# Optimization experiments

Hardware: AMD Instinct MI355X
Metric: run time of the kernel (lower is better)

Reference implementation:

```python
import jax, jax.numpy as jnp
import numpy as np

N_NODES = 100_000
N_EDGES = 1_600_000
N_GRAPHS = 2048
IN_CH, HID, EMB = 6, 64, 16
N_LIG, N_ADD, N_BASE, N_ARYL = 12, 23, 4, 16
TOTAL_IN = HID + 4 * EMB  # 128


def setup_inputs() -> dict:
    key = jax.random.key(0)
    ks = jax.random.split(key, 20)
    p = lambda k, shape: (jax.random.normal(k, shape, jnp.float32) * 0.05)
    return {
        "x": jax.random.normal(ks[0], (N_NODES, IN_CH), jnp.float32),
        "edge_index": jax.random.randint(ks[1], (2, N_EDGES), 0, N_NODES),
        "batch": jnp.sort(jax.random.randint(ks[2], (N_NODES,), 0, N_GRAPHS)),
        "ligand_idx": jax.random.randint(ks[3], (N_GRAPHS,), 0, N_LIG),
        "additive_idx": jax.random.randint(ks[4], (N_GRAPHS,), 0, N_ADD),
        "base_idx": jax.random.randint(ks[5], (N_GRAPHS,), 0, N_BASE),
        "aryl_idx": jax.random.randint(ks[6], (N_GRAPHS,), 0, N_ARYL),
        "emb_ligand": p(ks[7], (N_LIG, EMB)),
        "emb_additive": p(ks[8], (N_ADD, EMB)),
        "emb_base": p(ks[9], (N_BASE, EMB)),
        "emb_aryl": p(ks[10], (N_ARYL, EMB)),
        "W1": p(ks[11], (IN_CH, HID)),
        "b1": jnp.zeros((HID,), jnp.float32),
        "W2": p(ks[12], (HID, HID)),
        "b2": jnp.zeros((HID,), jnp.float32),
        "lin1_W": p(ks[13], (TOTAL_IN, HID)),
        "lin1_b": jnp.zeros((HID,), jnp.float32),
        "lin2_W": p(ks[14], (HID, 1)),
        "lin2_b": jnp.zeros((1,), jnp.float32),
    }


def gcn_conv(x, src, dst, W, b):
    """PyG GCNConv: add self-loops, sym-normalize, aggregate xW over edges."""
    n = x.shape[0]
    xw = x @ W  # [N, out]
    loop = jnp.arange(n)
    s = jnp.concatenate([src, loop])
    d = jnp.concatenate([dst, loop])
    deg = jax.ops.segment_sum(jnp.ones_like(d, dtype=xw.dtype), d, num_segments=n)
    dinv = jax.lax.rsqrt(jnp.maximum(deg, 1.0))  # deg >= 1 due to self-loops
    norm = (dinv[s] * dinv[d])[:, None]
    return jax.ops.segment_sum(xw[s] * norm, d, num_segments=n) + b


def reference(x, edge_index, batch, ligand_idx, additive_idx, base_idx, aryl_idx,
              emb_ligand, emb_additive, emb_base, emb_aryl,
              W1, b1, W2, b2, lin1_W, lin1_b, lin2_W, lin2_b):
    src, dst = edge_index[0], edge_index[1]
    h = jax.nn.relu(gcn_conv(x, src, dst, W1, b1))
    h = jax.nn.relu(gcn_conv(h, src, dst, W2, b2))
    # global mean pool over graphs
    sums = jax.ops.segment_sum(h, batch, num_segments=N_GRAPHS)
    cnt = jax.ops.segment_sum(jnp.ones((h.shape[0],), h.dtype), batch, num_segments=N_GRAPHS)
    pooled = sums / jnp.maximum(cnt, 1.0)[:, None]  # [G, HID]
    cat = jnp.concatenate([
        pooled,
        emb_ligand[ligand_idx], emb_additive[additive_idx],
        emb_base[base_idx], emb_aryl[aryl_idx],
    ], axis=-1)  # [G, HID + 4*EMB]
    hmid = jax.nn.relu(cat @ lin1_W + lin1_b)  # dropout is identity in eval mode
    return hmid @ lin2_W + lin2_b  # [G, 1]
```

## Files before the change

kernel.cpp:

```cpp
#include <hip/hip_runtime.h>
#include <hip/hip_bf16.h>

#define PCHUNK 4096
#define NBK 1024
#define BSZ 128
#define CAP 2560
#define CNT_STRIDE 16

__device__ inline float bf2f(unsigned int u16) { return __uint_as_float(u16 << 16); }
__device__ inline unsigned short f2bf(float f) {
    __hip_bfloat16 b = __float2bfloat16(f);
    return *(unsigned short*)&b;
}

typedef __attribute__((ext_vector_type(8))) short v8s;
typedef __attribute__((ext_vector_type(4))) float v4f;

__global__ void k_partition(const int* __restrict__ src, const int* __restrict__ dst, int E,
                            int* __restrict__ bucket_cnt, unsigned int* __restrict__ buckets,
                            float* __restrict__ zero_base, int zero_count) {
    __shared__ int hist[NBK];
    __shared__ int shift[NBK];
    __shared__ int cursor[NBK];
    __shared__ unsigned int staged_e[PCHUNK];
    __shared__ unsigned short staged_b[PCHUNK];
    __shared__ int wtot[4];
    int t = threadIdx.x;
    int lane = t & 63, wave = t >> 6;
    int base = blockIdx.x * PCHUNK;
    for (int i = blockIdx.x * 256 + t; i < zero_count; i += gridDim.x * 256)
        zero_base[i] = 0.f;
    for (int i = t; i < NBK; i += 256) hist[i] = 0;
    __syncthreads();
    int nE = E - base; if (nE > PCHUNK) nE = PCHUNK;
    for (int i = t; i < nE; i += 256) atomicAdd(&hist[dst[base + i] >> 7], 1);
    __syncthreads();
    int h0 = hist[4 * t], h1 = hist[4 * t + 1], h2 = hist[4 * t + 2], h3 = hist[4 * t + 3];
    int p1 = h0 + h1, p2 = p1 + h2, s = p2 + h3;
    int si = s;
    #pragma unroll
    for (int off = 1; off < 64; off <<= 1) {
        int u = __shfl_up(si, off, 64);
        if (lane >= off) si += u;
    }
    if (lane == 63) wtot[wave] = si;
    __syncthreads();
    int woff = 0;
    #pragma unroll
    for (int w2 = 0; w2 < 4; ++w2) woff += (w2 < wave) ? wtot[w2] : 0;
    int ebase = woff + si - s;
    int ex[4] = {ebase, ebase + h0, ebase + p1, ebase + p2};
    int cn[4] = {h0, h1, h2, h3};
    #pragma unroll
    for (int j = 0; j < 4; ++j) {
        int bidx = 4 * t + j;
        cursor[bidx] = ex[j];
        if (cn[j] > 0) {
            int g = atomicAdd(&bucket_cnt[bidx * CNT_STRIDE], cn[j]);
            shift[bidx] = g - ex[j];
        }
    }
    __syncthreads();
    for (int i = t; i < nE; i += 256) {
        int d = dst[base + i];
        int b = d >> 7;
        int r = atomicAdd(&cursor[b], 1);
        staged_e[r] = (unsigned int)src[base + i] | ((unsigned int)(d & (BSZ - 1)) << 24);
        staged_b[r] = (unsigned short)b;
    }
    __syncthreads();
    for (int i = t; i < nE; i += 256) {
        int b = staged_b[i];
        buckets[(size_t)b * CAP + shift[b] + i] = staged_e[i];
    }
}

__global__ void k_bucket_csr_xw1(const unsigned int* __restrict__ buckets,
                                 const int* __restrict__ bucket_cnt,
                                 int* __restrict__ offs, int* __restrict__ deg,
                                 float* __restrict__ dinv, int* __restrict__ csr,
                                 const float* __restrict__ x, const float* __restrict__ W1,
                                 unsigned short* __restrict__ A, int N) {
    __shared__ int dl[BSZ], cur[BSZ];
    __shared__ float dis[BSZ];
    __shared__ float W1s[6 * 64];
    __shared__ float xs[BSZ * 6];
    __shared__ int w0tot;
    int b = blockIdx.x, t = threadIdx.x;
    int nb0 = b * BSZ;
    for (int i = t; i < 6 * 64; i += 256) W1s[i] = W1[i];
    for (int i = t; i < BSZ * 6; i += 256) {
        int node = nb0 + i / 6;
        xs[i] = (node < N) ? x[(size_t)nb0 * 6 + i] : 0.f;
    }
    if (t < BSZ) dl[t] = 0;
    __syncthreads();
    int cnt = bucket_cnt[b * CNT_STRIDE];
    if (cnt > CAP) cnt = CAP;
    const unsigned int* bp = buckets + (size_t)b * CAP;
    for (int i = t; i < cnt; i += 256) atomicAdd(&dl[bp[i] >> 24], 1);
    __syncthreads();
    int lane = t & 63, wave = t >> 6;
    int v = (t < BSZ) ? dl[t] : 0;
    int si = v;
    #pragma unroll
    for (int off = 1; off < 64; off <<= 1) {
        int u = __shfl_up(si, off, 64);
        if (lane >= off) si += u;
    }
    if (t == 63) w0tot = si;
    __syncthreads();
    int ex = si - v + ((wave == 1) ? w0tot : 0);
    if (t < BSZ) {
        cur[t] = ex;
        float di = rsqrtf((float)v + 1.0f);
        dis[t] = di;
        int n = nb0 + t;
        if (n < N) { offs[n] = b * CAP + ex; deg[n] = v; dinv[n] = di; }
    }
    __syncthreads();
    int* cg = csr + (size_t)b * CAP;
    for (int i = t; i < cnt; i += 256) {
        unsigned int e = bp[i];
        int r = atomicAdd(&cur[e >> 24], 1);
        cg[r] = (int)(e & 0x00FFFFFFu);
    }
    int ch = t & 63, sub = t >> 6;
    for (int nl = sub; nl < BSZ; nl += 4) {
        int node = nb0 + nl;
        if (node < N) {
            float acc = 0.f;
            #pragma unroll
            for (int k = 0; k < 6; ++k) acc += xs[nl * 6 + k] * W1s[k * 64 + ch];
            A[(size_t)node * 64 + ch] = f2bf(acc * dis[nl]);
        }
    }
}

__global__ void k_pull1_xw2(const unsigned short* __restrict__ A, const int* __restrict__ csr,
                            const int* __restrict__ offs, const int* __restrict__ deg,
                            const float* __restrict__ dinv, const float* __restrict__ bias,
                            const float* __restrict__ W2, unsigned short* __restrict__ A2,
                            int N) {
    __shared__ unsigned short Ht[16][72];
    int t = threadIdx.x;
    int lane = t & 63, wave = t >> 6;
    int q = lane >> 4, m = lane & 15;
    int cbase = wave * 16;
    v8s b0h, b0l, b1h, b1l;
    #pragma unroll
    for (int j = 0; j < 8; ++j) {
        float w0 = W2[(q * 8 + j) * 64 + cbase + m];
        unsigned short h0 = f2bf(w0);
        b0h[j] = (short)h0;
        b0l[j] = (short)f2bf(w0 - bf2f(h0));
        float w1 = W2[(32 + q * 8 + j) * 64 + cbase + m];
        unsigned short h1 = f2bf(w1);
        b1h[j] = (short)h1;
        b1l[j] = (short)f2bf(w1 - bf2f(h1));
    }
    int n0 = blockIdx.x * 16;
    int nl = wave * 4 + q;
    int n = n0 + nl;
    bool valid = n < N;
    int nc = valid ? n : N - 1;
    int base = offs[nc];
    int dg = valid ? deg[nc] : 0;
    int dgm = dg, o;
    o = __shfl_xor(dgm, 16, 64); dgm = dgm > o ? dgm : o;
    o = __shfl_xor(dgm, 32, 64); dgm = dgm > o ? dgm : o;
    uint2 su = *(const uint2*)(A + ((size_t)nc << 6) + 4 * m);
    float a0 = __uint_as_float(su.x << 16);
    float a1 = __uint_as_float(su.x & 0xffff0000u);
    float a2 = __uint_as_float(su.y << 16);
    float a3 = __uint_as_float(su.y & 0xffff0000u);
    int i = 0;
    for (; i + 8 <= dgm; i += 8) {
        uint2 u[8];
        #pragma unroll
        for (int j = 0; j < 8; ++j) {
            unsigned int s = (unsigned int)csr[base + i + j];
            if (s >= (unsigned int)N) s = 0;
            u[j] = *(const uint2*)(A + ((size_t)s << 6) + 4 * m);
        }
        #pragma unroll
        for (int j = 0; j < 8; ++j) {
            unsigned int ux = (i + j < dg) ? u[j].x : 0u;
            unsigned int uy = (i + j < dg) ? u[j].y : 0u;
            a0 += __uint_as_float(ux << 16);
            a1 += __uint_as_float(ux & 0xffff0000u);
            a2 += __uint_as_float(uy << 16);
            a3 += __uint_as_float(uy & 0xffff0000u);
        }
    }
    for (; i < dgm; ++i) {
        unsigned int s = (unsigned int)csr[base + i];
        if (s >= (unsigned int)N) s = 0;
        uint2 uu = *(const uint2*)(A + ((size_t)s << 6) + 4 * m);
        unsigned int ux = (i < dg) ? uu.x : 0u;
        unsigned int uy = (i < dg) ? uu.y : 0u;
        a0 += __uint_as_float(ux << 16);
        a1 += __uint_as_float(ux & 0xffff0000u);
        a2 += __uint_as_float(uy << 16);
        a3 += __uint_as_float(uy & 0xffff0000u);
    }
    float di = valid ? dinv[n] : 0.f;
    float4 bb = *(const float4*)(bias + 4 * m);
    float v0 = fmaxf(fmaf(di, a0, bb.x), 0.f);
    float v1 = fmaxf(fmaf(di, a1, bb.y), 0.f);
    float v2 = fmaxf(fmaf(di, a2, bb.z), 0.f);
    float v3 = fmaxf(fmaf(di, a3, bb.w), 0.f);
    if (valid) {
        uint2 pk;
        pk.x = (unsigned int)f2bf(v0) | ((unsigned int)f2bf(v1) << 16);
        pk.y = (unsigned int)f2bf(v2) | ((unsigned int)f2bf(v3) << 16);
        *(uint2*)&Ht[nl][4 * m] = pk;
    }
    __syncthreads();
    union { uint4 u; v8s s; } a0u, a1u;
    a0u.u = *(const uint4*)&Ht[m][q * 8];
    a1u.u = *(const uint4*)&Ht[m][32 + q * 8];
    v4f acc = {0.f, 0.f, 0.f, 0.f};
    acc = __builtin_amdgcn_mfma_f32_16x16x32_bf16(a0u.s, b0l, acc, 0, 0, 0);
    acc = __builtin_amdgcn_mfma_f32_16x16x32_bf16(a1u.s, b1l, acc, 0, 0, 0);
    acc = __builtin_amdgcn_mfma_f32_16x16x32_bf16(a0u.s, b0h, acc, 0, 0, 0);
    acc = __builtin_amdgcn_mfma_f32_16x16x32_bf16(a1u.s, b1h, acc, 0, 0, 0);
    #pragma unroll
    for (int r = 0; r < 4; ++r) {
        int node = n0 + q * 4 + r;
        if (node < N)
            A2[(size_t)node * 64 + cbase + m] = f2bf(acc[r] * dinv[node]);
    }
}

__global__ void k_pull_pool(const unsigned short* __restrict__ A, const int* __restrict__ csr,
                            const int* __restrict__ offs, const int* __restrict__ deg,
                            const float* __restrict__ dinv, const float* __restrict__ bias,
                            const int* __restrict__ batch, float* __restrict__ pool, int N) {
    __shared__ float vt[4][4][64];
    int t = threadIdx.x;
    int lane = t & 63, wave = t >> 6;
    int q = lane >> 4, m = lane & 15;
    int n0 = blockIdx.x * 16;
    int nl = wave * 4 + q;
    int n = n0 + nl;
    bool valid = n < N;
    int nc = valid ? n : N - 1;
    int base = offs[nc];
    int dg = valid ? deg[nc] : 0;
    int dgm = dg, o;
    o = __shfl_xor(dgm, 16, 64); dgm = dgm > o ? dgm : o;
    o = __shfl_xor(dgm, 32, 64); dgm = dgm > o ? dgm : o;
    uint2 su = *(const uint2*)(A + ((size_t)nc << 6) + 4 * m);
    float a0 = __uint_as_float(su.x << 16);
    float a1 = __uint_as_float(su.x & 0xffff0000u);
    float a2 = __uint_as_float(su.y << 16);
    float a3 = __uint_as_float(su.y & 0xffff0000u);
    int i = 0;
    for (; i + 8 <= dgm; i += 8) {
        uint2 u[8];
        #pragma unroll
        for (int j = 0; j < 8; ++j) {
            unsigned int s = (unsigned int)csr[base + i + j];
            if (s >= (unsigned int)N) s = 0;
            u[j] = *(const uint2*)(A + ((size_t)s << 6) + 4 * m);
        }
        #pragma unroll
        for (int j = 0; j < 8; ++j) {
            unsigned int ux = (i + j < dg) ? u[j].x : 0u;
            unsigned int uy = (i + j < dg) ? u[j].y : 0u;
            a0 += __uint_as_float(ux << 16);
            a1 += __uint_as_float(ux & 0xffff0000u);
            a2 += __uint_as_float(uy << 16);
            a3 += __uint_as_float(uy & 0xffff0000u);
        }
    }
    for (; i < dgm; ++i) {
        unsigned int s = (unsigned int)csr[base + i];
        if (s >= (unsigned int)N) s = 0;
        uint2 uu = *(const uint2*)(A + ((size_t)s << 6) + 4 * m);
        unsigned int ux = (i < dg) ? uu.x : 0u;
        unsigned int uy = (i < dg) ? uu.y : 0u;
        a0 += __uint_as_float(ux << 16);
        a1 += __uint_as_float(ux & 0xffff0000u);
        a2 += __uint_as_float(uy << 16);
        a3 += __uint_as_float(uy & 0xffff0000u);
    }
    float di = valid ? dinv[n] : 0.f;
    float4 bb = *(const float4*)(bias + 4 * m);
    float4 vv;
    vv.x = fmaxf(fmaf(di, a0, bb.x), 0.f);
    vv.y = fmaxf(fmaf(di, a1, bb.y), 0.f);
    vv.z = fmaxf(fmaf(di, a2, bb.z), 0.f);
    vv.w = fmaxf(fmaf(di, a3, bb.w), 0.f);
    *(float4*)&vt[wave][q][4 * m] = vv;
    __syncthreads();
    int nw0 = n0 + wave * 4;
    #pragma unroll
    for (int r = 0; r < 4; ++r) {
        int nn = nw0 + r;
        if (nn < N) {
            float v = vt[wave][r][lane];
            atomicAdd(&pool[(size_t)batch[nn] * 64 + lane], v);
        }
    }
}

__global__ void k_final4(const float* __restrict__ pool, const int* __restrict__ batch,
                         int N, int G,
                         const int* __restrict__ lig, const int* __restrict__ add,
                         const int* __restrict__ base, const int* __restrict__ aryl,
                         const float* __restrict__ e_lig, const float* __restrict__ e_add,
                         const float* __restrict__ e_base, const float* __restrict__ e_aryl,
                         const float* __restrict__ lin1W, const float* __restrict__ lin1b,
                         const float* __restrict__ lin2W, const float* __restrict__ lin2b,
                         float* __restrict__ out) {
    __shared__ float Wl[128 * 64];
    __shared__ float cat[4][128];
    int t = threadIdx.x;
    int c = t & 63, wv = t >> 6;
    for (int i = t; i < 128 * 64; i += 256) Wl[i] = lin1W[i];
    int g = blockIdx.x * 4 + wv;
    if (g < G) {
        int res = 0;
        if (c < 2) {
            int target = g + c;
            int lo = 0, hi = N;
            while (lo < hi) {
                int mid = (lo + hi) >> 1;
                if (batch[mid] < target) lo = mid + 1; else hi = mid;
            }
            res = lo;
        }
        int lo = __shfl(res, 0, 64), hi = __shfl(res, 1, 64);
        float invc = 1.0f / fmaxf((float)(hi - lo), 1.0f);
        cat[wv][c] = pool[(size_t)g * 64 + c] * invc;
        float ev;
        if (c < 16)      ev = e_lig[lig[g] * 16 + c];
        else if (c < 32) ev = e_add[add[g] * 16 + (c - 16)];
        else if (c < 48) ev = e_base[base[g] * 16 + (c - 32)];
        else             ev = e_aryl[aryl[g] * 16 + (c - 48)];
        cat[wv][64 + c] = ev;
    }
    __syncthreads();
    if (g < G) {
        float acc = lin1b[c];
        #pragma unroll
        for (int k = 0; k < 128; ++k) acc += cat[wv][k] * Wl[k * 64 + c];
        float p = fmaxf(acc, 0.f) * lin2W[c];
        #pragma unroll
        for (int off = 32; off > 0; off >>= 1) p += __shfl_down(p, off, 64);
        if (c == 0) out[g] = p + lin2b[0];
    }
}

extern "C" void kernel_launch(void* const* d_in, const int* in_sizes, int n_in,
                              void* d_out, int out_size, void* d_ws, size_t ws_size,
                              hipStream_t stream) {
    const float* x      = (const float*)d_in[0];
    const int*   ei     = (const int*)d_in[1];
    const int*   batch  = (const int*)d_in[2];
    const int*   lig    = (const int*)d_in[3];
    const int*   addi   = (const int*)d_in[4];
    const int*   basei  = (const int*)d_in[5];
    const int*   aryl   = (const int*)d_in[6];
    const float* e_lig  = (const float*)d_in[7];
    const float* e_add  = (const float*)d_in[8];
    const float* e_base = (const float*)d_in[9];
    const float* e_aryl = (const float*)d_in[10];
    const float* W1     = (const float*)d_in[11];
    const float* b1     = (const float*)d_in[12];
    const float* W2     = (const float*)d_in[13];
    const float* b2     = (const float*)d_in[14];
    const float* lin1W  = (const float*)d_in[15];
    const float* lin1b  = (const float*)d_in[16];
    const float* lin2W  = (const float*)d_in[17];
    const float* lin2b  = (const float*)d_in[18];
    float* out = (float*)d_out;

    const int N = in_sizes[0] / 6;
    const int E = in_sizes[1] / 2;
    const int G = in_sizes[3];
    const int* src = ei;
    const int* dst = ei + E;
    const int NBb = (N + BSZ - 1) / BSZ;

    char* w = (char*)d_ws;
    size_t SA = (size_t)N * 64;
    unsigned short* A  = (unsigned short*)w;  w += SA * 2;
    unsigned short* A2 = (unsigned short*)w;  w += SA * 2;
    float* dinv = (float*)w;   w += (size_t)N * 4;
    int*   deg  = (int*)w;     w += (size_t)N * 4;
    int*   offs = (int*)w;     w += (size_t)N * 4;
    float* pool = (float*)w;   w += (size_t)G * 64 * 4;
    int* bucket_cnt = (int*)w; w += (size_t)NBK * CNT_STRIDE * 4;
    unsigned int* buckets = (unsigned int*)w;  w += (size_t)NBb * CAP * 4;
    int* csr    = (int*)w;     w += (size_t)NBb * CAP * 4;
    w += 4096;

    hipMemsetAsync(bucket_cnt, 0, (size_t)NBK * CNT_STRIDE * 4, stream);

    const int npart = (E + PCHUNK - 1) / PCHUNK;
    k_partition<<<npart, 256, 0, stream>>>(src, dst, E, bucket_cnt, buckets,
                                           pool, G * 64);
    k_bucket_csr_xw1<<<NBb, 256, 0, stream>>>(buckets, bucket_cnt,
                                              offs, deg, dinv, csr, x, W1, A, N);

    k_pull1_xw2<<<(N + 15) / 16, 256, 0, stream>>>(A, csr, offs, deg, dinv, b1, W2, A2, N);

    k_pull_pool<<<(N + 15) / 16, 256, 0, stream>>>(A2, csr, offs, deg, dinv, b2, batch, pool, N);

    k_final4<<<(G + 3) / 4, 256, 0, stream>>>(pool, batch, N, G, lig, addi, basei, aryl,
                                              e_lig, e_add, e_base, e_aryl,
                                              lin1W, lin1b, lin2W, lin2b, out);
}
```

Baseline: 246.8 us.

## Aggregate raw 6-channel features before applying W1 in first GCN layer

The first GCN layer now reorders aggregation and the linear transform. It gathers degree-scaled raw input features, padded to 8 floats per node, over neighbors, and applies W1, bias and ReLU after aggregation inside the pull kernel. This cuts the per-edge gather from 64 bf16 channels to 8 fp32 values, shrinking the random-access traffic in the first aggregation, and drops the A buffer write. In exchange each block handles 32 nodes, with an added LDS stage and a small per-node 6x64 matmul. Precision changes slightly because aggregation is now done in fp32 on raw features.

Result: faster. 222.4 us (median of 2 runs) (-9.9%).

```diff
diff --git a/kernel.cpp b/kernel.cpp
--- a/kernel.cpp
+++ b/kernel.cpp
@@ -75,20 +75,18 @@
     }
 }
 
-__global__ void k_bucket_csr_xw1(const unsigned int* __restrict__ buckets,
-                                 const int* __restrict__ bucket_cnt,
-                                 int* __restrict__ offs, int* __restrict__ deg,
-                                 float* __restrict__ dinv, int* __restrict__ csr,
-                                 const float* __restrict__ x, const float* __restrict__ W1,
-                                 unsigned short* __restrict__ A, int N) {
+__global__ void k_bucket_csr_xd(const unsigned int* __restrict__ buckets,
+                                const int* __restrict__ bucket_cnt,
+                                int* __restrict__ offs, int* __restrict__ deg,
+                                float* __restrict__ dinv, int* __restrict__ csr,
+                                const float* __restrict__ x,
+                                float* __restrict__ xd, int N) {
     __shared__ int dl[BSZ], cur[BSZ];
     __shared__ float dis[BSZ];
-    __shared__ float W1s[6 * 64];
     __shared__ float xs[BSZ * 6];
     __shared__ int w0tot;
     int b = blockIdx.x, t = threadIdx.x;
     int nb0 = b * BSZ;
-    for (int i = t; i < 6 * 64; i += 256) W1s[i] = W1[i];
     for (int i = t; i < BSZ * 6; i += 256) {
         int node = nb0 + i / 6;
         xs[i] = (node < N) ? x[(size_t)nb0 * 6 + i] : 0.f;
@@ -125,111 +123,103 @@
         int r = atomicAdd(&cur[e >> 24], 1);
         cg[r] = (int)(e & 0x00FFFFFFu);
     }
-    int ch = t & 63, sub = t >> 6;
-    for (int nl = sub; nl < BSZ; nl += 4) {
+    #pragma unroll
+    for (int j = 0; j < 4; ++j) {
+        int idx = t + j * 256;
+        int nl = idx >> 3, c = idx & 7;
         int node = nb0 + nl;
-        if (node < N) {
-            float acc = 0.f;
-            #pragma unroll
-            for (int k = 0; k < 6; ++k) acc += xs[nl * 6 + k] * W1s[k * 64 + ch];
-            A[(size_t)node * 64 + ch] = f2bf(acc * dis[nl]);
-        }
-    }
-}
-
-__global__ void k_pull1_xw2(const unsigned short* __restrict__ A, const int* __restrict__ csr,
+        if (node < N)
+            xd[((size_t)node << 3) + c] = (c < 6) ? xs[nl * 6 + c] * dis[nl] : 0.f;
+    }
+}
+
+__global__ void k_pull1_xw2(const float* __restrict__ xd, const int* __restrict__ csr,
                             const int* __restrict__ offs, const int* __restrict__ deg,
-                            const float* __restrict__ dinv, const float* __restrict__ bias,
+                            const float* __restrict__ dinv,
+                            const float* __restrict__ W1, const float* __restrict__ b1,
                             const float* __restrict__ W2, unsigned short* __restrict__ A2,
                             int N) {
-    __shared__ unsigned short Ht[16][72];
+    __shared__ float agg6[32][8];
+    __shared__ unsigned short Ht[32][72];
+    __shared__ float W1s[6 * 64];
     int t = threadIdx.x;
     int lane = t & 63, wave = t >> 6;
-    int q = lane >> 4, m = lane & 15;
+    int q = lane >> 4, m16 = lane & 15;
     int cbase = wave * 16;
+    for (int i = t; i < 6 * 64; i += 256) W1s[i] = W1[i];
     v8s b0h, b0l, b1h, b1l;
     #pragma unroll
     for (int j = 0; j < 8; ++j) {
-        float w0 = W2[(q * 8 + j) * 64 + cbase + m];
+        float w0 = W2[(q * 8 + j) * 64 + cbase + m16];
         unsigned short h0 = f2bf(w0);
         b0h[j] = (short)h0;
         b0l[j] = (short)f2bf(w0 - bf2f(h0));
-        float w1 = W2[(32 + q * 8 + j) * 64 + cbase + m];
+        float w1 = W2[(32 + q * 8 + j) * 64 + cbase + m16];
         unsigned short h1 = f2bf(w1);
         b1h[j] = (short)h1;
         b1l[j] = (short)f2bf(w1 - bf2f(h1));
     }
-    int n0 = blockIdx.x * 16;
-    int nl = wave * 4 + q;
+    int n0 = blockIdx.x * 32;
+    int oct = lane >> 3, m = lane & 7;
+    int nl = wave * 8 + oct;
     int n = n0 + nl;
     bool valid = n < N;
     int nc = valid ? n : N - 1;
     int base = offs[nc];
     int dg = valid ? deg[nc] : 0;
     int dgm = dg, o;
+    o = __shfl_xor(dgm, 8, 64);  dgm = dgm > o ? dgm : o;
     o = __shfl_xor(dgm, 16, 64); dgm = dgm > o ? dgm : o;
     o = __shfl_xor(dgm, 32, 64); dgm = dgm > o ? dgm : o;
-    uint2 su = *(const uint2*)(A + ((size_t)nc << 6) + 4 * m);
-    float a0 = __uint_as_float(su.x << 16);
-    float a1 = __uint_as_float(su.x & 0xffff0000u);
-    float a2 = __uint_as_float(su.y << 16);
-    float a3 = __uint_as_float(su.y & 0xffff0000u);
+    float a = xd[((size_t)nc << 3) + m];
     int i = 0;
     for (; i + 8 <= dgm; i += 8) {
-        uint2 u[8];
+        float u[8];
         #pragma unroll
         for (int j = 0; j < 8; ++j) {
             unsigned int s = (unsigned int)csr[base + i + j];
             if (s >= (unsigned int)N) s = 0;
-            u[j] = *(const uint2*)(A + ((size_t)s << 6) + 4 * m);
-        }
-        #pragma unroll
-        for (int j = 0; j < 8; ++j) {
-            unsigned int ux = (i + j < dg) ? u[j].x : 0u;
-            unsigned int uy = (i + j < dg) ? u[j].y : 0u;
-            a0 += __uint_as_float(ux << 16);
-            a1 += __uint_as_float(ux & 0xffff0000u);
-            a2 += __uint_as_float(uy << 16);
-            a3 += __uint_as_float(uy & 0xffff0000u);
-        }
+            u[j] = xd[((size_t)s << 3) + m];
+        }
+        #pragma unroll
+        for (int j = 0; j < 8; ++j)
+            a += (i + j < dg) ? u[j] : 0.f;
     }
     for (; i < dgm; ++i) {
         unsigned int s = (unsigned int)csr[base + i];
         if (s >= (unsigned int)N) s = 0;
-        uint2 uu = *(const uint2*)(A + ((size_t)s << 6) + 4 * m);
-        unsigned int ux = (i < dg) ? uu.x : 0u;
-        unsigned int uy = (i < dg) ? uu.y : 0u;
-        a0 += __uint_as_float(ux << 16);
-        a1 += __uint_as_float(ux & 0xffff0000u);
-        a2 += __uint_as_float(uy << 16);
-        a3 += __uint_as_float(uy & 0xffff0000u);
-    }
-    float di = valid ? dinv[n] : 0.f;
-    float4 bb = *(const float4*)(bias + 4 * m);
-    float v0 = fmaxf(fmaf(di, a0, bb.x), 0.f);
-    float v1 = fmaxf(fmaf(di, a1, bb.y), 0.f);
-    float v2 = fmaxf(fmaf(di, a2, bb.z), 0.f);
-    float v3 = fmaxf(fmaf(di, a3, bb.w), 0.f);
-    if (valid) {
-        uint2 pk;
-        pk.x = (unsigned int)f2bf(v0) | ((unsigned int)f2bf(v1) << 16);
-        pk.y = (unsigned int)f2bf(v2) | ((unsigned int)f2bf(v3) << 16);
-        *(uint2*)&Ht[nl][4 * m] = pk;
-    }
-    __syncthreads();
-    union { uint4 u; v8s s; } a0u, a1u;
-    a0u.u = *(const uint4*)&Ht[m][q * 8];
-    a1u.u = *(const uint4*)&Ht[m][32 + q * 8];
-    v4f acc = {0.f, 0.f, 0.f, 0.f};
-    acc = __builtin_amdgcn_mfma_f32_16x16x32_bf16(a0u.s, b0l, acc, 0, 0, 0);
-    acc = __builtin_amdgcn_mfma_f32_16x16x32_bf16(a1u.s, b1l, acc, 0, 0, 0);
-    acc = __builtin_amdgcn_mfma_f32_16x16x32_bf16(a0u.s, b0h, acc, 0, 0, 0);
-    acc = __builtin_amdgcn_mfma_f32_16x16x32_bf16(a1u.s, b1h, acc, 0, 0, 0);
-    #pragma unroll
-    for (int r = 0; r < 4; ++r) {
-        int node = n0 + q * 4 + r;
-        if (node < N)
-            A2[(size_t)node * 64 + cbase + m] = f2bf(acc[r] * dinv[node]);
+        float u = xd[((size_t)s << 3) + m];
+        a += (i < dg) ? u : 0.f;
+    }
+    agg6[nl][m] = (valid ? dinv[n] : 0.f) * a;
+    __syncthreads();
+    float bl = b1[lane];
+    #pragma unroll
+    for (int r = 0; r < 8; ++r) {
+        int node_l = wave * 8 + r;
+        float acc = bl;
+        #pragma unroll
+        for (int k = 0; k < 6; ++k) acc += agg6[node_l][k] * W1s[k * 64 + lane];
+        Ht[node_l][lane] = f2bf(fmaxf(acc, 0.f));
+    }
+    __syncthreads();
+    #pragma unroll
+    for (int tile = 0; tile < 2; ++tile) {
+        int row = tile * 16 + m16;
+        union { uint4 u; v8s s; } a0u, a1u;
+        a0u.u = *(const uint4*)&Ht[row][q * 8];
+        a1u.u = *(const uint4*)&Ht[row][32 + q * 8];
+        v4f acc = {0.f, 0.f, 0.f, 0.f};
+        acc = __builtin_amdgcn_mfma_f32_16x16x32_bf16(a0u.s, b0l, acc, 0, 0, 0);
+        acc = __builtin_amdgcn_mfma_f32_16x16x32_bf16(a1u.s, b1l, acc, 0, 0, 0);
+        acc = __builtin_amdgcn_mfma_f32_16x16x32_bf16(a0u.s, b0h, acc, 0, 0, 0);
+        acc = __builtin_amdgcn_mfma_f32_16x16x32_bf16(a1u.s, b1h, acc, 0, 0, 0);
+        #pragma unroll
+        for (int r = 0; r < 4; ++r) {
+            int node = n0 + tile * 16 + q * 4 + r;
+            if (node < N)
+                A2[(size_t)node * 64 + cbase + m16] = f2bf(acc[r] * dinv[node]);
+        }
     }
 }
 
@@ -387,7 +377,7 @@
 
     char* w = (char*)d_ws;
     size_t SA = (size_t)N * 64;
-    unsigned short* A  = (unsigned short*)w;  w += SA * 2;
+    float* xd = (float*)w;     w += (size_t)N * 8 * 4;
     unsigned short* A2 = (unsigned short*)w;  w += SA * 2;
     float* dinv = (float*)w;   w += (size_t)N * 4;
     int*   deg  = (int*)w;     w += (size_t)N * 4;
@@ -403,10 +393,11 @@
     const int npart = (E + PCHUNK - 1) / PCHUNK;
     k_partition<<<npart, 256, 0, stream>>>(src, dst, E, bucket_cnt, buckets,
                                            pool, G * 64);
-    k_bucket_csr_xw1<<<NBb, 256, 0, stream>>>(buckets, bucket_cnt,
-                                              offs, deg, dinv, csr, x, W1, A, N);
-
-    k_pull1_xw2<<<(N + 15) / 16, 256, 0, stream>>>(A, csr, offs, deg, dinv, b1, W2, A2, N);
+    k_bucket_csr_xd<<<NBb, 256, 0, stream>>>(buckets, bucket_cnt,
+                                             offs, deg, dinv, csr, x, xd, N);
+
+    k_pull1_xw2<<<(N + 31) / 32, 256, 0, stream>>>(xd, csr, offs, deg, dinv,
+                                                   W1, b1, W2, A2, N);
 
     k_pull_pool<<<(N + 15) / 16, 256, 0, stream>>>(A2, csr, offs, deg, dinv, b2, batch, pool, N);
 
```
